# Kernel optimization log

Measured on AMD Instinct MI355X. Metric: run time of the kernel, lower is better.

## Reference

```python
import jax, jax.numpy as jnp
import numpy as np

B, C, H, W = 8, 320, 64, 64      # query feature map
S_KV, D_KV = 77, 1024            # key/value (text) tokens
HEADS, DIM_HEAD = 8, 64
INNER = HEADS * DIM_HEAD         # 512


def setup_inputs() -> dict:
    key = jax.random.key(0)
    ks = jax.random.split(key, 7)
    return {
        "query": jax.random.normal(ks[0], (B, C, H, W), dtype=jnp.float32),
        "key_value": jax.random.normal(ks[1], (B, S_KV, D_KV), dtype=jnp.float32),
        "Wq": jax.random.normal(ks[2], (C, INNER), dtype=jnp.float32) * (C ** -0.5),
        "Wk": jax.random.normal(ks[3], (D_KV, INNER), dtype=jnp.float32) * (D_KV ** -0.5),
        "Wv": jax.random.normal(ks[4], (D_KV, INNER), dtype=jnp.float32) * (D_KV ** -0.5),
        "Wo": jax.random.normal(ks[5], (INNER, C), dtype=jnp.float32) * (INNER ** -0.5),
        "bo": jnp.zeros((C,), dtype=jnp.float32),
    }


def reference(query, key_value, Wq, Wk, Wv, Wo, bo):
    b, c, h, w = query.shape
    n = h * w
    # [B,C,H,W] -> [B,N,C]
    q_flat = query.reshape(b, c, n).transpose(0, 2, 1)
    # projections, then split heads: [B, S, heads, dim_head]
    q = (q_flat @ Wq).reshape(b, n, HEADS, DIM_HEAD)
    k = (key_value @ Wk).reshape(b, S_KV, HEADS, DIM_HEAD)
    v = (key_value @ Wv).reshape(b, S_KV, HEADS, DIM_HEAD)
    scale = DIM_HEAD ** -0.5
    # attn logits: [B, heads, N, S_kv]
    logits = jnp.einsum('bnhd,bshd->bhns', q, k) * scale
    attn = jax.nn.softmax(logits, axis=-1)
    # weighted values -> merge heads: [B, N, inner]
    out = jnp.einsum('bhns,bshd->bnhd', attn, v).reshape(b, n, INNER)
    out = out @ Wo + bo  # dropout p=0.0 is identity
    # [B,N,C] -> [B,C,H,W]
    return out.transpose(0, 2, 1).reshape(b, c, h, w)
```

## Files before the change

### kernel.cpp

```cpp
#include <hip/hip_runtime.h>
#include <hip/hip_bf16.h>

#define BB     8
#define CC     320
#define NN     4096
#define SKV    77
#define DKV    1024
#define HEADS  8
#define DH     64
#define INNER  512
#define SCALE  0.125f

typedef float f32x4  __attribute__((ext_vector_type(4)));
typedef short bf16x8 __attribute__((ext_vector_type(8)));
typedef short s16x4  __attribute__((ext_vector_type(4)));

static __device__ __forceinline__ short f2bf(float f) {
  unsigned u = __float_as_uint(f);
  return (short)((u + 0x7fffu + ((u >> 16) & 1u)) >> 16);
}

__global__ __launch_bounds__(256) void prep_kernel(
    const float* __restrict__ kv, const float* __restrict__ Wk,
    const float* __restrict__ Wv, const float* __restrict__ Wq,
    const float* __restrict__ Wo, short* __restrict__ kv_bf,
    short* __restrict__ Wk_t, short* __restrict__ Wv_t,
    short* __restrict__ Wq_t, short* __restrict__ Wo_t,
    unsigned* __restrict__ zero_base) {
  const int blk = blockIdx.x, t = threadIdx.x;
  if (blk < 616) {
    const int base = blk * 1024;
    #pragma unroll
    for (int i = 0; i < 4; ++i) kv_bf[base + i*256 + t] = f2bf(kv[base + i*256 + t]);
  } else if (blk < 1128) {
    const int n = blk - 616;
    for (int k = t; k < 1024; k += 256) Wk_t[n*1024 + k] = f2bf(Wk[k*512 + n]);
  } else if (blk < 1640) {
    const int n = blk - 1128;
    for (int k = t; k < 1024; k += 256) Wv_t[n*1024 + k] = f2bf(Wv[k*512 + n]);
  } else if (blk < 2152) {
    const int n = blk - 1640;
    for (int c = t; c < 320; c += 256) Wq_t[n*320 + c] = f2bf(Wq[c*512 + n]);
  } else if (blk < 2472) {
    const int c = blk - 2152;
    for (int j = t; j < 512; j += 256) Wo_t[c*512 + j] = f2bf(Wo[j*320 + c]);
  } else {
    const int base = (blk - 2472) * 1024;
    #pragma unroll
    for (int i = 0; i < 4; ++i) zero_base[base + i*256 + t] = 0u;
  }
}

__global__ __launch_bounds__(256) void kvproj_kernel(
    const short* __restrict__ kv_bf, const short* __restrict__ Wk_t,
    const short* __restrict__ Wv_t, short* __restrict__ K_ws,
    short* __restrict__ V_ws) {
  const int t = threadIdx.x, w = t >> 6, lane = t & 63;
  const int l15 = lane & 15, q = lane >> 4;
  const int m0 = (blockIdx.x * 4 + w) * 16;
  const int y = blockIdx.y;
  const bool isK = (y < 8);
  const int h = y & 7;
  const short* __restrict__ Wt = isK ? Wk_t : Wv_t;
  const int arow = (m0 + l15 < 616) ? (m0 + l15) : 615;

  const f32x4 z = {0.f, 0.f, 0.f, 0.f};
  f32x4 acc[4] = {z, z, z, z};
  for (int k0 = 0; k0 < 1024; k0 += 32) {
    const bf16x8 a = *(const bf16x8*)(kv_bf + arow*1024 + k0 + q*8);
    #pragma unroll
    for (int nt = 0; nt < 4; ++nt) {
      const int n = h*64 + nt*16 + l15;
      const bf16x8 bfr = *(const bf16x8*)(Wt + n*1024 + k0 + q*8);
      acc[nt] = __builtin_amdgcn_mfma_f32_16x16x32_bf16(a, bfr, acc[nt], 0, 0, 0);
    }
  }
  #pragma unroll
  for (int nt = 0; nt < 4; ++nt) {
    const int d = nt*16 + l15;
    #pragma unroll
    for (int r = 0; r < 4; ++r) {
      const int row = m0 + q*4 + r;
      if (row < 616) {
        const int b = (int)(((unsigned)row * 54472u) >> 22);
        const int s = row - b*77;
        if (isK) K_ws[((b*8 + h)*80 + s)*64 + d] = f2bf(acc[nt][r]);
        else     V_ws[((b*8 + h)*64 + d)*96 + s] = f2bf(acc[nt][r]);
      }
    }
  }
}

__global__ __launch_bounds__(256) void qproj_kernel(
    const float* __restrict__ query, const short* __restrict__ Wq_t,
    short* __restrict__ Q_ws) {
  const int bx = blockIdx.x;
  const int b = bx >> 6;
  const int n0 = (bx & 63) * 64;
  const int t = threadIdx.x, w = t >> 6, lane = t & 63;
  const int l15 = lane & 15, q = lane >> 4;
  __shared__ short X_lds[64 * 328];

  {
    const int tok = t & 63, cbase = t >> 6;
    for (int i = 0; i < 80; ++i) {
      const int c = cbase + i*4;
      X_lds[tok*328 + c] = f2bf(query[((size_t)(b*CC + c))*NN + n0 + tok]);
    }
  }
  __syncthreads();

  const f32x4 z = {0.f, 0.f, 0.f, 0.f};
  f32x4 acc[4][8];
  #pragma unroll
  for (int mt = 0; mt < 4; ++mt)
    #pragma unroll
    for (int nt = 0; nt < 8; ++nt) acc[mt][nt] = z;

  const int nbase = w * 128;
  for (int k0 = 0; k0 < 320; k0 += 32) {
    bf16x8 a[4];
    #pragma unroll
    for (int mt = 0; mt < 4; ++mt)
      a[mt] = *(const bf16x8*)(X_lds + (mt*16 + l15)*328 + k0 + q*8);
    #pragma unroll
    for (int nt = 0; nt < 8; ++nt) {
      const int n = nbase + nt*16 + l15;
      const bf16x8 bfr = *(const bf16x8*)(Wq_t + n*320 + k0 + q*8);
      #pragma unroll
      for (int mt = 0; mt < 4; ++mt)
        acc[mt][nt] = __builtin_amdgcn_mfma_f32_16x16x32_bf16(a[mt], bfr, acc[mt][nt], 0, 0, 0);
    }
  }

  short* outst = X_lds;
  for (int half = 0; half < 2; ++half) {
    __syncthreads();
    if ((w >> 1) == half) {
      const int ch = (w & 1) * 128;
      #pragma unroll
      for (int mt = 0; mt < 4; ++mt)
        #pragma unroll
        for (int nt = 0; nt < 8; ++nt)
          #pragma unroll
          for (int r = 0; r < 4; ++r)
            outst[(mt*16 + q*4 + r)*264 + ch + nt*16 + l15] = f2bf(acc[mt][nt][r]);
    }
    __syncthreads();
    const int tok = t >> 2, c0 = (t & 3) * 64;
    const short* lsrc = outst + tok*264 + c0;
    short* gdst = Q_ws + ((size_t)(b*NN + n0 + tok))*512 + half*256 + c0;
    #pragma unroll
    for (int i = 0; i < 8; ++i)
      *(bf16x8*)(gdst + i*8) = *(const bf16x8*)(lsrc + i*8);
  }
}

__global__ __launch_bounds__(256) void attn_kernel(
    const short* __restrict__ Q_ws, const short* __restrict__ K_ws,
    const short* __restrict__ V_ws, const short* __restrict__ Wo_t,
    const float* __restrict__ bo, float* __restrict__ out) {
  const int n0 = blockIdx.x * 64;
  const int b  = blockIdx.y;
  const int t = threadIdx.x, w = t >> 6, lane = t & 63;
  const int l15 = lane & 15, q = lane >> 4;

  __shared__ short k_lds[80 * 72];
  __shared__ short v_lds[64 * 104];
  __shared__ short o_lds[64 * 72];
  __shared__ short p_lds[4 * 16 * 104];
  short* pw = p_lds + w * 16 * 104;

  for (int i = lane; i < 832; i += 64) ((unsigned*)pw)[i] = 0u;

  const f32x4 z = {0.f, 0.f, 0.f, 0.f};
  f32x4 outacc[5][4];
  #pragma unroll
  for (int mt = 0; mt < 5; ++mt)
    #pragma unroll
    for (int nt = 0; nt < 4; ++nt) outacc[mt][nt] = z;

  for (int h = 0; h < HEADS; ++h) {
    {
      const short* Ksrc = K_ws + (size_t)(b*8 + h) * 80 * 64;
      #pragma unroll
      for (int i = 0; i < 5; ++i) {
        const int idx4 = (i*256 + t) * 4;
        const int s = idx4 >> 6, d = idx4 & 63;
        *(s16x4*)(k_lds + s*72 + d) = *(const s16x4*)(Ksrc + idx4);
      }
      const short* Vsrc = V_ws + (size_t)(b*8 + h) * 64 * 96;
      const int row = t >> 2;
      #pragma unroll
      for (int i = 0; i < 6; ++i) {
        const int col = (t & 3) * 24 + i * 4;
        *(s16x4*)(v_lds + row*104 + col) = *(const s16x4*)(Vsrc + row*96 + col);
      }
    }
    __syncthreads();

    f32x4 qk[5] = {z, z, z, z, z};
    const short* Qrow = Q_ws + ((size_t)(b*NN + n0 + w*16 + l15))*512 + h*64;
    #pragma unroll
    for (int ks = 0; ks < 2; ++ks) {
      const bf16x8 bq = *(const bf16x8*)(Qrow + ks*32 + q*8);
      #pragma unroll
      for (int mt = 0; mt < 5; ++mt) {
        const bf16x8 a = *(const bf16x8*)(k_lds + (mt*16 + l15)*72 + ks*32 + q*8);
        qk[mt] = __builtin_amdgcn_mfma_f32_16x16x32_bf16(a, bq, qk[mt], 0, 0, 0);
      }
    }

    float mx = -1e30f;
    #pragma unroll
    for (int mt = 0; mt < 5; ++mt)
      #pragma unroll
      for (int r = 0; r < 4; ++r) {
        const int s = mt*16 + q*4 + r;
        const float vv = (s < 77) ? qk[mt][r] * SCALE : -1e30f;
        qk[mt][r] = vv;
        mx = fmaxf(mx, vv);
      }
    mx = fmaxf(mx, __shfl_xor(mx, 16));
    mx = fmaxf(mx, __shfl_xor(mx, 32));
    float sum = 0.f;
    #pragma unroll
    for (int mt = 0; mt < 5; ++mt)
      #pragma unroll
      for (int r = 0; r < 4; ++r) {
        const int s = mt*16 + q*4 + r;
        const float e = (s < 77) ? __expf(qk[mt][r] - mx) : 0.f;
        qk[mt][r] = e;
        sum += e;
      }
    sum += __shfl_xor(sum, 16);
    sum += __shfl_xor(sum, 32);
    const float inv = 1.0f / sum;
    #pragma unroll
    for (int mt = 0; mt < 5; ++mt)
      #pragma unroll
      for (int r = 0; r < 4; ++r) {
        const int s = mt*16 + q*4 + r;
        if (s < 77) pw[l15*104 + s] = f2bf(qk[mt][r] * inv);
      }

    f32x4 ov[4] = {z, z, z, z};
    #pragma unroll
    for (int ks = 0; ks < 3; ++ks) {
      const bf16x8 bp = *(const bf16x8*)(pw + l15*104 + ks*32 + q*8);
      #pragma unroll
      for (int mt = 0; mt < 4; ++mt) {
        const bf16x8 a = *(const bf16x8*)(v_lds + (mt*16 + l15)*104 + ks*32 + q*8);
        ov[mt] = __builtin_amdgcn_mfma_f32_16x16x32_bf16(a, bp, ov[mt], 0, 0, 0);
      }
    }
    #pragma unroll
    for (int mt = 0; mt < 4; ++mt)
      #pragma unroll
      for (int r = 0; r < 4; ++r)
        o_lds[(w*16 + l15)*72 + mt*16 + q*4 + r] = f2bf(ov[mt][r]);
    __syncthreads();

    #pragma unroll
    for (int ks = 0; ks < 2; ++ks) {
      bf16x8 bfrag[4];
      #pragma unroll
      for (int nt = 0; nt < 4; ++nt)
        bfrag[nt] = *(const bf16x8*)(o_lds + (nt*16 + l15)*72 + ks*32 + q*8);
      #pragma unroll
      for (int mt = 0; mt < 5; ++mt) {
        const int c = w*80 + mt*16 + l15;
        const bf16x8 a = *(const bf16x8*)(Wo_t + c*512 + h*64 + ks*32 + q*8);
        #pragma unroll
        for (int nt = 0; nt < 4; ++nt)
          outacc[mt][nt] = __builtin_amdgcn_mfma_f32_16x16x32_bf16(a, bfrag[nt], outacc[mt][nt], 0, 0, 0);
      }
    }
  }

  #pragma unroll
  for (int mt = 0; mt < 5; ++mt)
    #pragma unroll
    for (int r = 0; r < 4; ++r) {
      const int c = w*80 + mt*16 + q*4 + r;
      const float bv = bo[c];
      #pragma unroll
      for (int nt = 0; nt < 4; ++nt)
        out[((size_t)(b*CC + c))*NN + n0 + nt*16 + l15] = outacc[mt][nt][r] + bv;
    }
}

extern "C" void kernel_launch(void* const* d_in, const int* in_sizes, int n_in,
                              void* d_out, int out_size, void* d_ws, size_t ws_size,
                              hipStream_t stream) {
  const float* query = (const float*)d_in[0];
  const float* kv    = (const float*)d_in[1];
  const float* Wq    = (const float*)d_in[2];
  const float* Wk    = (const float*)d_in[3];
  const float* Wv    = (const float*)d_in[4];
  const float* Wo    = (const float*)d_in[5];
  const float* bo    = (const float*)d_in[6];
  float* out = (float*)d_out;

  char* p = (char*)d_ws;
  short* K_ws  = (short*)(p);
  short* V_ws  = (short*)(p +   819200);
  short* Q_ws  = (short*)(p +  1802240);
  short* kv_bf = (short*)(p + 35356672);
  short* Wk_t  = (short*)(p + 36618240);
  short* Wv_t  = (short*)(p + 37666816);
  short* Wq_t  = (short*)(p + 38715392);
  short* Wo_t  = (short*)(p + 39043072);

  prep_kernel<<<2912, 256, 0, stream>>>(kv, Wk, Wv, Wq, Wo, kv_bf, Wk_t, Wv_t,
                                        Wq_t, Wo_t, (unsigned*)p);
  kvproj_kernel<<<dim3(10, 16), 256, 0, stream>>>(kv_bf, Wk_t, Wv_t, K_ws, V_ws);
  qproj_kernel<<<512, 256, 0, stream>>>(query, Wq_t, Q_ws);
  attn_kernel<<<dim3(64, 8), 256, 0, stream>>>(Q_ws, K_ws, V_ws, Wo_t, bo, out);
}
```

Baseline: 209.8 us.

## Fuse Q projection into attention kernel and tile K/V weight transposes

The separate Q-projection kernel and its bf16 Q workspace round trip are removed. Each attention block now converts its query tile to bf16 in LDS, keeps the X fragments in registers, and computes each head's Q slice with MFMA against Wq_t before QK^T. The Wk/Wv transposes in the prep kernel are also rewritten as 64x64 LDS-tiled transposes to make the global accesses coalesced. In exchange, the attention kernel takes on extra MFMA work, extra register pressure from the X fragments, and an additional barrier per head.

```diff
diff --git a/kernel.cpp b/kernel.cpp
--- a/kernel.cpp
+++ b/kernel.cpp
@@ -10,14 +10,27 @@
 #define DH     64
 #define INNER  512
 #define SCALE  0.125f
+#define XSTR   330
 
 typedef float f32x4  __attribute__((ext_vector_type(4)));
 typedef short bf16x8 __attribute__((ext_vector_type(8)));
 typedef short s16x4  __attribute__((ext_vector_type(4)));
+typedef short s16x2  __attribute__((ext_vector_type(2)));
 
 static __device__ __forceinline__ short f2bf(float f) {
   unsigned u = __float_as_uint(f);
   return (short)((u + 0x7fffu + ((u >> 16) & 1u)) >> 16);
+}
+
+static __device__ __forceinline__ bf16x8 ld_frag4(const short* p) {
+  const s16x2 a = *(const s16x2*)(p);
+  const s16x2 b = *(const s16x2*)(p + 2);
+  const s16x2 c = *(const s16x2*)(p + 4);
+  const s16x2 d = *(const s16x2*)(p + 6);
+  bf16x8 r;
+  r[0]=a[0]; r[1]=a[1]; r[2]=b[0]; r[3]=b[1];
+  r[4]=c[0]; r[5]=c[1]; r[6]=d[0]; r[7]=d[1];
+  return r;
 }
 
 __global__ __launch_bounds__(256) void prep_kernel(
@@ -27,25 +40,39 @@
     short* __restrict__ Wk_t, short* __restrict__ Wv_t,
     short* __restrict__ Wq_t, short* __restrict__ Wo_t,
     unsigned* __restrict__ zero_base) {
+  __shared__ float T[64 * 65];
   const int blk = blockIdx.x, t = threadIdx.x;
   if (blk < 616) {
     const int base = blk * 1024;
     #pragma unroll
     for (int i = 0; i < 4; ++i) kv_bf[base + i*256 + t] = f2bf(kv[base + i*256 + t]);
-  } else if (blk < 1128) {
-    const int n = blk - 616;
-    for (int k = t; k < 1024; k += 256) Wk_t[n*1024 + k] = f2bf(Wk[k*512 + n]);
-  } else if (blk < 1640) {
-    const int n = blk - 1128;
-    for (int k = t; k < 1024; k += 256) Wv_t[n*1024 + k] = f2bf(Wv[k*512 + n]);
-  } else if (blk < 2152) {
-    const int n = blk - 1640;
+  } else if (blk < 872) {
+    const int tile = blk - 616;
+    const bool isK = tile < 128;
+    const int tt = isK ? tile : tile - 128;
+    const int kt = tt >> 3, ct = tt & 7;
+    const float* __restrict__ src = isK ? Wk : Wv;
+    short* __restrict__ dst = isK ? Wk_t : Wv_t;
+    const int cl = t & 63, rb = t >> 6;
+    #pragma unroll
+    for (int i = 0; i < 16; ++i) {
+      const int r = rb + i*4;
+      T[r*65 + cl] = src[(size_t)(kt*64 + r)*512 + ct*64 + cl];
+    }
+    __syncthreads();
+    #pragma unroll
+    for (int i = 0; i < 16; ++i) {
+      const int nl = rb + i*4;
+      dst[(size_t)(ct*64 + nl)*1024 + kt*64 + cl] = f2bf(T[cl*65 + nl]);
+    }
+  } else if (blk < 1384) {
+    const int n = blk - 872;
     for (int c = t; c < 320; c += 256) Wq_t[n*320 + c] = f2bf(Wq[c*512 + n]);
-  } else if (blk < 2472) {
-    const int c = blk - 2152;
+  } else if (blk < 1704) {
+    const int c = blk - 1384;
     for (int j = t; j < 512; j += 256) Wo_t[c*512 + j] = f2bf(Wo[j*320 + c]);
   } else {
-    const int base = (blk - 2472) * 1024;
+    const int base = (blk - 1704) * 1024;
     #pragma unroll
     for (int i = 0; i < 4; ++i) zero_base[base + i*256 + t] = 0u;
   }
@@ -91,85 +118,39 @@
   }
 }
 
-__global__ __launch_bounds__(256) void qproj_kernel(
+__global__ __launch_bounds__(256, 2) void attn_kernel(
     const float* __restrict__ query, const short* __restrict__ Wq_t,
-    short* __restrict__ Q_ws) {
-  const int bx = blockIdx.x;
-  const int b = bx >> 6;
-  const int n0 = (bx & 63) * 64;
-  const int t = threadIdx.x, w = t >> 6, lane = t & 63;
-  const int l15 = lane & 15, q = lane >> 4;
-  __shared__ short X_lds[64 * 328];
-
-  {
-    const int tok = t & 63, cbase = t >> 6;
-    for (int i = 0; i < 80; ++i) {
-      const int c = cbase + i*4;
-      X_lds[tok*328 + c] = f2bf(query[((size_t)(b*CC + c))*NN + n0 + tok]);
-    }
-  }
-  __syncthreads();
-
-  const f32x4 z = {0.f, 0.f, 0.f, 0.f};
-  f32x4 acc[4][8];
-  #pragma unroll
-  for (int mt = 0; mt < 4; ++mt)
-    #pragma unroll
-    for (int nt = 0; nt < 8; ++nt) acc[mt][nt] = z;
-
-  const int nbase = w * 128;
-  for (int k0 = 0; k0 < 320; k0 += 32) {
-    bf16x8 a[4];
-    #pragma unroll
-    for (int mt = 0; mt < 4; ++mt)
-      a[mt] = *(const bf16x8*)(X_lds + (mt*16 + l15)*328 + k0 + q*8);
-    #pragma unroll
-    for (int nt = 0; nt < 8; ++nt) {
-      const int n = nbase + nt*16 + l15;
-      const bf16x8 bfr = *(const bf16x8*)(Wq_t + n*320 + k0 + q*8);
-      #pragma unroll
-      for (int mt = 0; mt < 4; ++mt)
-        acc[mt][nt] = __builtin_amdgcn_mfma_f32_16x16x32_bf16(a[mt], bfr, acc[mt][nt], 0, 0, 0);
-    }
-  }
-
-  short* outst = X_lds;
-  for (int half = 0; half < 2; ++half) {
-    __syncthreads();
-    if ((w >> 1) == half) {
-      const int ch = (w & 1) * 128;
-      #pragma unroll
-      for (int mt = 0; mt < 4; ++mt)
-        #pragma unroll
-        for (int nt = 0; nt < 8; ++nt)
-          #pragma unroll
-          for (int r = 0; r < 4; ++r)
-            outst[(mt*16 + q*4 + r)*264 + ch + nt*16 + l15] = f2bf(acc[mt][nt][r]);
-    }
-    __syncthreads();
-    const int tok = t >> 2, c0 = (t & 3) * 64;
-    const short* lsrc = outst + tok*264 + c0;
-    short* gdst = Q_ws + ((size_t)(b*NN + n0 + tok))*512 + half*256 + c0;
-    #pragma unroll
-    for (int i = 0; i < 8; ++i)
-      *(bf16x8*)(gdst + i*8) = *(const bf16x8*)(lsrc + i*8);
-  }
-}
-
-__global__ __launch_bounds__(256) void attn_kernel(
-    const short* __restrict__ Q_ws, const short* __restrict__ K_ws,
-    const short* __restrict__ V_ws, const short* __restrict__ Wo_t,
-    const float* __restrict__ bo, float* __restrict__ out) {
+    const short* __restrict__ K_ws, const short* __restrict__ V_ws,
+    const short* __restrict__ Wo_t, const float* __restrict__ bo,
+    float* __restrict__ out) {
   const int n0 = blockIdx.x * 64;
   const int b  = blockIdx.y;
   const int t = threadIdx.x, w = t >> 6, lane = t & 63;
   const int l15 = lane & 15, q = lane >> 4;
 
-  __shared__ short k_lds[80 * 72];
-  __shared__ short v_lds[64 * 104];
-  __shared__ short o_lds[64 * 72];
-  __shared__ short p_lds[4 * 16 * 104];
+  __shared__ short smem[28288];
+  short* k_lds = smem;
+  short* v_lds = smem + 5760;
+  short* o_lds = smem + 12416;
+  short* p_lds = smem + 17024;
+  short* q_lds = smem + 23680;
+  short* X_lds = smem;
   short* pw = p_lds + w * 16 * 104;
+  short* qw = q_lds + w * 16 * 72;
+
+  {
+    const int tok = t & 63, cb = t >> 6;
+    for (int i = 0; i < 80; ++i) {
+      const int c = cb + i*4;
+      X_lds[tok*XSTR + c] = f2bf(query[((size_t)(b*CC + c))*NN + n0 + tok]);
+    }
+  }
+  __syncthreads();
+  bf16x8 xf[10];
+  #pragma unroll
+  for (int kk = 0; kk < 10; ++kk)
+    xf[kk] = ld_frag4(X_lds + (w*16 + l15)*XSTR + kk*32 + q*8);
+  __syncthreads();
 
   for (int i = lane; i < 832; i += 64) ((unsigned*)pw)[i] = 0u;
 
@@ -181,6 +162,7 @@
     for (int nt = 0; nt < 4; ++nt) outacc[mt][nt] = z;
 
   for (int h = 0; h < HEADS; ++h) {
+    if (h) __syncthreads();
     {
       const short* Ksrc = K_ws + (size_t)(b*8 + h) * 80 * 64;
       #pragma unroll
@@ -199,11 +181,25 @@
     }
     __syncthreads();
 
+    f32x4 qa[4] = {z, z, z, z};
+    #pragma unroll
+    for (int kk = 0; kk < 10; ++kk) {
+      #pragma unroll
+      for (int nt = 0; nt < 4; ++nt) {
+        const bf16x8 bfr = *(const bf16x8*)(Wq_t + (h*64 + nt*16 + l15)*320 + kk*32 + q*8);
+        qa[nt] = __builtin_amdgcn_mfma_f32_16x16x32_bf16(xf[kk], bfr, qa[nt], 0, 0, 0);
+      }
+    }
+    #pragma unroll
+    for (int nt = 0; nt < 4; ++nt)
+      #pragma unroll
+      for (int r = 0; r < 4; ++r)
+        qw[(q*4 + r)*72 + nt*16 + l15] = f2bf(qa[nt][r]);
+
     f32x4 qk[5] = {z, z, z, z, z};
-    const short* Qrow = Q_ws + ((size_t)(b*NN + n0 + w*16 + l15))*512 + h*64;
     #pragma unroll
     for (int ks = 0; ks < 2; ++ks) {
-      const bf16x8 bq = *(const bf16x8*)(Qrow + ks*32 + q*8);
+      const bf16x8 bq = *(const bf16x8*)(qw + l15*72 + ks*32 + q*8);
       #pragma unroll
       for (int mt = 0; mt < 5; ++mt) {
         const bf16x8 a = *(const bf16x8*)(k_lds + (mt*16 + l15)*72 + ks*32 + q*8);
@@ -305,16 +301,14 @@
   char* p = (char*)d_ws;
   short* K_ws  = (short*)(p);
   short* V_ws  = (short*)(p +   819200);
-  short* Q_ws  = (short*)(p +  1802240);
-  short* kv_bf = (short*)(p + 35356672);
-  short* Wk_t  = (short*)(p + 36618240);
-  short* Wv_t  = (short*)(p + 37666816);
-  short* Wq_t  = (short*)(p + 38715392);
-  short* Wo_t  = (short*)(p + 39043072);
-
-  prep_kernel<<<2912, 256, 0, stream>>>(kv, Wk, Wv, Wq, Wo, kv_bf, Wk_t, Wv_t,
+  short* kv_bf = (short*)(p +  1802240);
+  short* Wk_t  = (short*)(p +  3063808);
+  short* Wv_t  = (short*)(p +  4112384);
+  short* Wq_t  = (short*)(p +  5160960);
+  short* Wo_t  = (short*)(p +  5488640);
+
+  prep_kernel<<<2144, 256, 0, stream>>>(kv, Wk, Wv, Wq, Wo, kv_bf, Wk_t, Wv_t,
                                         Wq_t, Wo_t, (unsigned*)p);
   kvproj_kernel<<<dim3(10, 16), 256, 0, stream>>>(kv_bf, Wk_t, Wv_t, K_ws, V_ws);
-  qproj_kernel<<<512, 256, 0, stream>>>(query, Wq_t, Q_ws);
-  attn_kernel<<<dim3(64, 8), 256, 0, stream>>>(Q_ws, K_ws, V_ws, Wo_t, bo, out);
-}
+  attn_kernel<<<dim3(64, 8), 256, 0, stream>>>(query, Wq_t, K_ws, V_ws, Wo_t, bo, out);
+}
```

Result: slower. 224.8 us (+7.2%).
